# Kernel optimization log

Measured on AMD Instinct MI355X. Metric: run time of the kernel, lower is better.

The kernel has to match this reference:

```python
import jax, jax.numpy as jnp
import numpy as np


def setup_inputs() -> dict:
    key = jax.random.key(0)
    ks = jax.random.split(key, 8)
    B, L, D = 8, 4096, 1024
    s = 1.0 / np.sqrt(D)  # torch Linear default init scale (approx)
    return {
        "x": jax.random.normal(ks[0], (B, L, D), dtype=jnp.float32),
        "hidden": jax.random.normal(ks[1], (B, D), dtype=jnp.float32),
        "W_f": jax.random.normal(ks[2], (D, D), dtype=jnp.float32) * s,
        "b_f": jnp.zeros((D,), dtype=jnp.float32),
        "W_i": jax.random.normal(ks[3], (D, D), dtype=jnp.float32) * s,
        "b_i": jnp.zeros((D,), dtype=jnp.float32),
        "W_o": jax.random.normal(ks[4], (D, D), dtype=jnp.float32) * s,
        "b_o": jnp.zeros((D,), dtype=jnp.float32),
    }


def reference(x, hidden, W_f, b_f, W_i, b_i, W_o, b_o):
    # x: [B, L, D], hidden: [B, D]
    D = x.shape[-1]
    lin = jnp.linspace(0.0, 1.0, D, dtype=x.dtype)  # per-channel gate scale
    remember = jax.nn.sigmoid(jnp.einsum('bld,ed->ble', x, W_f) + b_f) * lin
    forget = 1.0 - remember
    inp = jnp.tanh(jnp.einsum('bld,ed->ble', x, W_i) + b_i) * remember

    # linear recurrence h_t = forget_t * h_{t-1} + inp_t  via parallel scan
    def combine(c1, c2):
        a1, u1 = c1
        a2, u2 = c2
        return (a1 * a2, a2 * u1 + u2)

    cumprod_forget, h_inner = jax.lax.associative_scan(combine, (forget, inp), axis=1)
    h = h_inner + hidden[:, None, :] * cumprod_forget  # inject initial hidden state
    y = jnp.einsum('bld,ed->ble', h, W_o) + b_o
    return y, h
```

## Files before the change

kernel.cpp:

```cpp
#include <hip/hip_runtime.h>
#include <stdint.h>

#define B_ 8
#define L_ 4096
#define D_ 1024
#define M_ (B_*L_)
#define CHUNKS 64
#define TCH (L_/CHUNKS)

typedef float f32x4 __attribute__((ext_vector_type(4)));
typedef float f32x2 __attribute__((ext_vector_type(2)));
typedef short short8 __attribute__((ext_vector_type(8)));
typedef unsigned short ushort4v __attribute__((ext_vector_type(4)));

static __device__ __forceinline__ unsigned short f2bf(float f) {
  union { float f; unsigned u; } v; v.f = f;
  unsigned r = v.u + 0x7FFFu + ((v.u >> 16) & 1u);
  return (unsigned short)(r >> 16);
}
static __device__ __forceinline__ float bf2f(unsigned short u) {
  union { unsigned u; float f; } v; v.u = ((unsigned)u) << 16; return v.f;
}

#define GLOAD16(g, l) \
  __builtin_amdgcn_global_load_lds((__attribute__((address_space(1))) const void*)(g), \
                                   (__attribute__((address_space(3))) void*)(l), 16, 0, 0)

__global__ __launch_bounds__(256)
void cvt_bf16(const float* __restrict__ src, unsigned short* __restrict__ dst, int n8)
{
  int gid = blockIdx.x * 256 + threadIdx.x;
  if (gid >= n8) return;
  const f32x4* s = (const f32x4*)(src + (size_t)gid * 8);
  f32x4 v0 = s[0], v1 = s[1];
  union { short8 v; unsigned short u[8]; } w;
  w.u[0] = f2bf(v0[0]); w.u[1] = f2bf(v0[1]); w.u[2] = f2bf(v0[2]); w.u[3] = f2bf(v0[3]);
  w.u[4] = f2bf(v1[0]); w.u[5] = f2bf(v1[1]); w.u[6] = f2bf(v1[2]); w.u[7] = f2bf(v1[3]);
  *(short8*)(dst + (size_t)gid * 8) = w.v;
}

template<int OBF>
__global__ __launch_bounds__(512, 2)
void gemm256(const unsigned short* __restrict__ A,
             const unsigned short* __restrict__ Bw,
             const float* __restrict__ bias,
             float* __restrict__ outf,
             unsigned short* __restrict__ outb)
{
  __shared__ unsigned short lds[65536];
  char* ldsb = (char*)lds;

  const int tid  = threadIdx.x;
  const int lane = tid & 63;
  const int wid  = tid >> 6;
  const int wm   = wid >> 2;
  const int wn   = wid & 3;
  const int frow = lane & 15, ks = lane >> 4;
  const int xsw  = (ks ^ ((frow >> 1) & 3)) << 4;

  const int nwg = gridDim.x;
  const int wg  = (blockIdx.x & 7) * (nwg >> 3) + (blockIdx.x >> 3);
  const int bm  = (wg & 127) * 256;
  const int bn  = (wg >> 7) * 256;

  const int r0  = tid >> 2;
  const int scl = ((tid & 3) ^ ((r0 >> 1) & 3)) << 4;
  const char* pA = (const char*)A  + (size_t)(bm + r0) * 2048 + scl;
  const char* pB = (const char*)Bw + (size_t)(bn + r0) * 2048 + scl;
  const int dst16 = tid * 16;

  f32x4 acc[8][4] = {};
  short8 aq[4], bq[4];

  auto stgA = [&](int T, int kk, int buf) {
    const char* s = pA + T * 128 + kk * 64;
    char* d = ldsb + buf * 32768 + kk * 16384 + dst16;
    GLOAD16(s, d);
    GLOAD16(s + (size_t)128 * 2048, d + 8192);
  };
  auto stgB = [&](int T, int kk, int buf) {
    const char* s = pB + T * 128 + kk * 64;
    char* d = ldsb + 65536 + buf * 32768 + kk * 16384 + dst16;
    GLOAD16(s, d);
    GLOAD16(s + (size_t)128 * 2048, d + 8192);
  };
  auto ldA4 = [&](const char* LA, int kk, int ih) {
    const char* base = LA + kk * 16384 + (wm * 128 + ih * 64 + frow) * 64 + xsw;
    aq[0] = *(const short8*)(base);
    aq[1] = *(const short8*)(base + 1024);
    aq[2] = *(const short8*)(base + 2048);
    aq[3] = *(const short8*)(base + 3072);
  };
  auto ldB4 = [&](const char* LB, int kk) {
    const char* base = LB + kk * 16384 + (wn * 64 + frow) * 64 + xsw;
    bq[0] = *(const short8*)(base);
    bq[1] = *(const short8*)(base + 1024);
    bq[2] = *(const short8*)(base + 2048);
    bq[3] = *(const short8*)(base + 3072);
  };
  auto mfma16 = [&](int ih) {
    __builtin_amdgcn_s_setprio(1);
    #pragma unroll
    for (int i2 = 0; i2 < 4; ++i2) {
      #pragma unroll
      for (int j = 0; j < 4; ++j)
        acc[ih * 4 + i2][j] =
          __builtin_amdgcn_mfma_f32_16x16x32_bf16(aq[i2], bq[j], acc[ih * 4 + i2][j], 0, 0, 0);
    }
    __builtin_amdgcn_s_setprio(0);
  };

  stgA(0, 0, 0); stgB(0, 0, 0);
  stgA(0, 1, 0); stgB(0, 1, 0);
  stgA(1, 0, 1); stgB(1, 0, 1);
  asm volatile("s_waitcnt vmcnt(8)" ::: "memory");
  __builtin_amdgcn_s_barrier();

  for (int t = 0; t < 16; ++t) {
    const int buf = t & 1;
    const char* LA = ldsb + buf * 32768;
    const char* LB = ldsb + 65536 + buf * 32768;
    ldB4(LB, 0);
    ldA4(LA, 0, 0);
    if (t < 15) stgA(t + 1, 1, (t + 1) & 1);
    __builtin_amdgcn_s_barrier();
    asm volatile("s_waitcnt lgkmcnt(0)" ::: "memory");
    mfma16(0);
    __builtin_amdgcn_s_barrier();
    ldA4(LA, 0, 1);
    if (t < 15) stgB(t + 1, 1, (t + 1) & 1);
    if (t < 15) asm volatile("s_waitcnt vmcnt(8)" ::: "memory");
    else        asm volatile("s_waitcnt vmcnt(0)" ::: "memory");
    __builtin_amdgcn_s_barrier();
    asm volatile("s_waitcnt lgkmcnt(0)" ::: "memory");
    mfma16(1);
    __builtin_amdgcn_s_barrier();
    ldB4(LB, 1);
    ldA4(LA, 1, 0);
    if (t < 14) stgA(t + 2, 0, buf);
    __builtin_amdgcn_s_barrier();
    asm volatile("s_waitcnt lgkmcnt(0)" ::: "memory");
    mfma16(0 + 4 - 4);
    __builtin_amdgcn_s_barrier();
    ldA4(LA, 1, 1);
    if (t < 14) stgB(t + 2, 0, buf);
    if (t < 14) asm volatile("s_waitcnt vmcnt(8)" ::: "memory");
    else        asm volatile("s_waitcnt vmcnt(4)" ::: "memory");
    __builtin_amdgcn_s_barrier();
    asm volatile("s_waitcnt lgkmcnt(0)" ::: "memory");
    mfma16(1);
    __builtin_amdgcn_s_barrier();
  }

  float bv[4];
  #pragma unroll
  for (int j = 0; j < 4; ++j) bv[j] = bias[bn + wn * 64 + j * 16 + frow];
  #pragma unroll
  for (int ii = 0; ii < 8; ++ii) {
    int row = bm + wm * 128 + ii * 16 + ks * 4;
    #pragma unroll
    for (int j = 0; j < 4; ++j) {
      int col = bn + wn * 64 + j * 16 + frow;
      #pragma unroll
      for (int r = 0; r < 4; ++r) {
        float v = acc[ii][j][r] + bv[j];
        if constexpr (OBF) outb[(size_t)(row + r) * D_ + col] = f2bf(v);
        else               outf[(size_t)(row + r) * D_ + col] = v;
      }
    }
  }
}

static __device__ __forceinline__ void gate1(float zf, float zi, float lin,
                                             float& f, float& inp)
{
  float rem = lin / (1.0f + __expf(-zf));
  float ez  = __expf(2.0f * zi);
  float th  = 1.0f - 2.0f / (ez + 1.0f);
  f = 1.0f - rem;
  inp = th * rem;
}

__global__ __launch_bounds__(256)
void scan_partial_b(const unsigned short* __restrict__ zf,
                    const unsigned short* __restrict__ zi,
                    float* __restrict__ Ag, float* __restrict__ Ug)
{
  int blk = blockIdx.x;
  int b = blk >> 6, c = blk & 63;
  int e = threadIdx.x << 2;
  float lin0 = (float)e * (1.0f / 1023.0f);
  size_t base = ((size_t)b * L_ + (size_t)c * TCH) * D_ + e;
  f32x4 a = {1.f,1.f,1.f,1.f}, u = {0.f,0.f,0.f,0.f};
  for (int t = 0; t < TCH; ++t) {
    ushort4v f4 = *(const ushort4v*)(zf + base + (size_t)t * D_);
    ushort4v i4 = *(const ushort4v*)(zi + base + (size_t)t * D_);
    #pragma unroll
    for (int j = 0; j < 4; ++j) {
      float fg, inp;
      gate1(bf2f(f4[j]), bf2f(i4[j]), lin0 + (float)j * (1.0f/1023.0f), fg, inp);
      u[j] = fmaf(fg, u[j], inp);
      a[j] *= fg;
    }
  }
  size_t o = (size_t)(b * CHUNKS + c) * D_ + e;
  *(f32x4*)(Ag + o) = a;
  *(f32x4*)(Ug + o) = u;
}

__global__ __launch_bounds__(256)
void scan_carry(const float* __restrict__ Ag, const float* __restrict__ Ug,
                const float* __restrict__ hidden, float* __restrict__ Hin)
{
  int gid = blockIdx.x * 256 + threadIdx.x;
  int b = gid >> 8;
  int e = (gid & 255) << 2;
  f32x4 h = *(const f32x4*)(hidden + (size_t)b * D_ + e);
  for (int c = 0; c < CHUNKS; ++c) {
    size_t o = (size_t)(b * CHUNKS + c) * D_ + e;
    *(f32x4*)(Hin + o) = h;
    f32x4 A = *(const f32x4*)(Ag + o);
    f32x4 U = *(const f32x4*)(Ug + o);
    h = A * h + U;
  }
}

__global__ __launch_bounds__(256)
void scan_apply_b(const unsigned short* __restrict__ zf,
                  const unsigned short* __restrict__ zi,
                  const float* __restrict__ Hin,
                  float* __restrict__ hout, unsigned short* __restrict__ hb)
{
  int blk = blockIdx.x;
  int b = blk >> 6, c = blk & 63;
  int e = threadIdx.x << 2;
  float lin0 = (float)e * (1.0f / 1023.0f);
  size_t base = ((size_t)b * L_ + (size_t)c * TCH) * D_ + e;
  f32x4 h = *(const f32x4*)(Hin + (size_t)(b * CHUNKS + c) * D_ + e);
  for (int t = 0; t < TCH; ++t) {
    size_t o = base + (size_t)t * D_;
    ushort4v f4 = *(const ushort4v*)(zf + o);
    ushort4v i4 = *(const ushort4v*)(zi + o);
    #pragma unroll
    for (int j = 0; j < 4; ++j) {
      float fg, inp;
      gate1(bf2f(f4[j]), bf2f(i4[j]), lin0 + (float)j * (1.0f/1023.0f), fg, inp);
      h[j] = fmaf(fg, h[j], inp);
    }
    *(f32x4*)(hout + o) = h;
    ushort4v p;
    p[0] = f2bf(h[0]); p[1] = f2bf(h[1]); p[2] = f2bf(h[2]); p[3] = f2bf(h[3]);
    *(ushort4v*)(hb + o) = p;
  }
}

template<int MODE>
__global__ __launch_bounds__(256, 2)
void gemm_slow(const float* __restrict__ A, const float* __restrict__ B0,
               const float* __restrict__ B1, const float* __restrict__ bias0,
               const float* __restrict__ bias1, float* __restrict__ out0,
               float* __restrict__ out1)
{
  constexpr int BK = 32;
  __shared__ unsigned short As[128 * BK];
  __shared__ unsigned short Bs0[128 * BK];
  __shared__ unsigned short Bs1[(MODE == 0) ? (128 * BK) : 8];

  const int tid = threadIdx.x, lane = tid & 63, wave = tid >> 6;
  const int wr = wave >> 1, wc = wave & 1;
  const int bm = blockIdx.x * 128, bn = blockIdx.y * 128;
  f32x4 acc0[4][4] = {};
  f32x4 acc1[(MODE == 0) ? 4 : 1][(MODE == 0) ? 4 : 1] = {};
  const int frow = lane & 15, kslot = lane >> 4;
  const int xs = kslot ^ (frow & 3);

  auto stage = [&](const float* src, unsigned short* dst) {
    #pragma unroll
    for (int p = 0; p < 4; ++p) {
      int g = p * 256 + tid;
      int row = g >> 3, kq = (g & 7) << 2;
      f32x4 v = *(const f32x4*)(src + (size_t)row * D_ + kq);
      ushort4v w;
      w[0] = f2bf(v[0]); w[1] = f2bf(v[1]); w[2] = f2bf(v[2]); w[3] = f2bf(v[3]);
      int byte = kq << 1, slot = byte >> 4, sub = byte & 15;
      int off = row * 64 + ((slot ^ (row & 3)) << 4) + sub;
      *(ushort4v*)((char*)dst + off) = w;
    }
  };

  for (int k0 = 0; k0 < D_; k0 += BK) {
    stage(A + (size_t)bm * D_ + k0, As);
    stage(B0 + (size_t)bn * D_ + k0, Bs0);
    if constexpr (MODE == 0) stage(B1 + (size_t)bn * D_ + k0, Bs1);
    __syncthreads();
    short8 af[4], bf0[4], bf1[4];
    #pragma unroll
    for (int i = 0; i < 4; ++i) {
      int ar = wr * 64 + i * 16 + frow;
      af[i] = *(const short8*)((const char*)As + ar * 64 + (xs << 4));
      int br = wc * 64 + i * 16 + frow;
      bf0[i] = *(const short8*)((const char*)Bs0 + br * 64 + (xs << 4));
      if constexpr (MODE == 0)
        bf1[i] = *(const short8*)((const char*)Bs1 + br * 64 + (xs << 4));
    }
    #pragma unroll
    for (int i = 0; i < 4; ++i)
      #pragma unroll
      for (int j = 0; j < 4; ++j) {
        acc0[i][j] = __builtin_amdgcn_mfma_f32_16x16x32_bf16(af[i], bf0[j], acc0[i][j], 0, 0, 0);
        if constexpr (MODE == 0)
          acc1[i][j] = __builtin_amdgcn_mfma_f32_16x16x32_bf16(af[i], bf1[j], acc1[i][j], 0, 0, 0);
      }
    __syncthreads();
  }
  #pragma unroll
  for (int i = 0; i < 4; ++i)
    #pragma unroll
    for (int j = 0; j < 4; ++j)
      #pragma unroll
      for (int r = 0; r < 4; ++r) {
        int row = bm + wr * 64 + i * 16 + (lane >> 4) * 4 + r;
        int col = bn + wc * 64 + j * 16 + (lane & 15);
        size_t idx = (size_t)row * D_ + col;
        if constexpr (MODE == 0) {
          float zf = acc0[i][j][r] + bias0[col];
          float linv = (float)col * (1.0f / 1023.0f);
          float rem = linv / (1.0f + __expf(-zf));
          float zi = acc1[i][j][r] + bias1[col];
          float e2 = __expf(2.0f * zi);
          float th = 1.0f - 2.0f / (e2 + 1.0f);
          out0[idx] = 1.0f - rem;
          out1[idx] = th * rem;
        } else {
          out0[idx] = acc0[i][j][r] + bias0[col];
        }
      }
}

__global__ __launch_bounds__(256)
void scan_partial_f(const float* __restrict__ p0, const float* __restrict__ p1,
                    float* __restrict__ Ag, float* __restrict__ Ug)
{
  int blk = blockIdx.x;
  int b = blk >> 7;
  int c = (blk >> 1) & (CHUNKS - 1);
  int e = ((blk & 1) << 9) + threadIdx.x * 2;
  size_t base = ((size_t)b * L_ + (size_t)c * TCH) * D_ + e;
  f32x2 a = {1.0f, 1.0f}, u = {0.0f, 0.0f};
  for (int t = 0; t < TCH; ++t) {
    f32x2 f = *(const f32x2*)(p0 + base + (size_t)t * D_);
    f32x2 i = *(const f32x2*)(p1 + base + (size_t)t * D_);
    u = f * u + i;
    a = a * f;
  }
  size_t o = (size_t)(b * CHUNKS + c) * D_ + e;
  *(f32x2*)(Ag + o) = a;
  *(f32x2*)(Ug + o) = u;
}

__global__ __launch_bounds__(256)
void scan_apply_f(const float* __restrict__ p0, float* __restrict__ p1_io,
                  const float* __restrict__ Hin)
{
  int blk = blockIdx.x;
  int b = blk >> 7;
  int c = (blk >> 1) & (CHUNKS - 1);
  int e = ((blk & 1) << 9) + threadIdx.x * 2;
  size_t base = ((size_t)b * L_ + (size_t)c * TCH) * D_ + e;
  f32x2 h = *(const f32x2*)(Hin + (size_t)(b * CHUNKS + c) * D_ + e);
  for (int t = 0; t < TCH; ++t) {
    size_t o = base + (size_t)t * D_;
    f32x2 f = *(const f32x2*)(p0 + o);
    f32x2 i = *(const f32x2*)(p1_io + o);
    h = f * h + i;
    *(f32x2*)(p1_io + o) = h;
  }
}

extern "C" void kernel_launch(void* const* d_in, const int* in_sizes, int n_in,
                              void* d_out, int out_size, void* d_ws, size_t ws_size,
                              hipStream_t stream)
{
  const float* x      = (const float*)d_in[0];
  const float* hidden = (const float*)d_in[1];
  const float* W_f    = (const float*)d_in[2];
  const float* b_f    = (const float*)d_in[3];
  const float* W_i    = (const float*)d_in[4];
  const float* b_i    = (const float*)d_in[5];
  const float* W_o    = (const float*)d_in[6];
  const float* b_o    = (const float*)d_in[7];

  float* y = (float*)d_out;
  float* h = y + (size_t)M_ * D_;

  const size_t xb_elems = (size_t)M_ * D_;
  const size_t w_elems  = (size_t)D_ * D_;
  const size_t agg      = (size_t)B_ * CHUNKS * D_;
  const size_t need = (xb_elems * 3 + 3 * w_elems) * 2 + agg * 3 * 4;

  if (ws_size >= need) {
    unsigned short* xb  = (unsigned short*)d_ws;
    unsigned short* wfb = xb + xb_elems;
    unsigned short* wib = wfb + w_elems;
    unsigned short* wob = wib + w_elems;
    unsigned short* zfb = wob + w_elems;
    unsigned short* zib = zfb + xb_elems;
    float* Ag  = (float*)(zib + xb_elems);
    float* Ug  = Ag + agg;
    float* Hin = Ug + agg;

    cvt_bf16<<<(int)(xb_elems / 8 / 256), 256, 0, stream>>>(x,   xb,  (int)(xb_elems / 8));
    cvt_bf16<<<(int)(w_elems / 8 / 256), 256, 0, stream>>>(W_f, wfb, (int)(w_elems / 8));
    cvt_bf16<<<(int)(w_elems / 8 / 256), 256, 0, stream>>>(W_i, wib, (int)(w_elems / 8));
    cvt_bf16<<<(int)(w_elems / 8 / 256), 256, 0, stream>>>(W_o, wob, (int)(w_elems / 8));

    int gblocks = (M_ / 256) * (D_ / 256);
    gemm256<1><<<gblocks, 512, 0, stream>>>(xb, wfb, b_f, nullptr, zfb);
    gemm256<1><<<gblocks, 512, 0, stream>>>(xb, wib, b_i, nullptr, zib);

    int pblocks = B_ * CHUNKS;
    scan_partial_b<<<pblocks, 256, 0, stream>>>(zfb, zib, Ag, Ug);
    scan_carry<<<(B_ * D_ / 4) / 256, 256, 0, stream>>>(Ag, Ug, hidden, Hin);
    scan_apply_b<<<pblocks, 256, 0, stream>>>(zfb, zib, Hin, h, xb);

    gemm256<0><<<gblocks, 512, 0, stream>>>(xb, wob, b_o, y, nullptr);
  } else {
    float* Ag  = (float*)d_ws;
    float* Ug  = Ag + agg;
    float* Hin = Ug + agg;
    dim3 gg(M_ / 128, D_ / 128);
    int pblocks = B_ * CHUNKS * 2;

    gemm_slow<0><<<gg, 256, 0, stream>>>(x, W_f, W_i, b_f, b_i, y, h);
    scan_partial_f<<<pblocks, 256, 0, stream>>>(y, h, Ag, Ug);
    scan_carry<<<(B_ * D_ / 4) / 256, 256, 0, stream>>>(Ag, Ug, hidden, Hin);
    scan_apply_f<<<pblocks, 256, 0, stream>>>(y, h, Hin);
    gemm_slow<1><<<gg, 256, 0, stream>>>(h, W_o, nullptr, b_o, nullptr, y, nullptr);
  }
}
```

Before: 423.7 us.

## Fuse forget/input GEMMs into one N=2048 GEMM, remap tiles, double scan chunks

The two input-projection GEMMs become a single launch over a concatenated W_f|W_i weight, with each tile writing to the zf or zi plane. x is read once and the output N width doubles. Block-to-tile mapping is redone so each XCD handles a contiguous group of M rows across all N columns, aiming for better L2 reuse. The three weight conversions are merged into one kernel, and the scan chunk count goes from 64 to 128 to give the scan kernels more parallelism. The catch is that the workspace must now hold the three bf16 weights contiguously, and there are more carry steps in the sequential carry kernel.

```diff
diff --git a/kernel.cpp b/kernel.cpp
--- a/kernel.cpp
+++ b/kernel.cpp
@@ -5,7 +5,7 @@
 #define L_ 4096
 #define D_ 1024
 #define M_ (B_*L_)
-#define CHUNKS 64
+#define CHUNKS 128
 #define TCH (L_/CHUNKS)
 
 typedef float f32x4 __attribute__((ext_vector_type(4)));
@@ -39,13 +39,31 @@
   *(short8*)(dst + (size_t)gid * 8) = w.v;
 }
 
-template<int OBF>
+__global__ __launch_bounds__(256)
+void cvt_w3(const float* __restrict__ w0, const float* __restrict__ w1,
+            const float* __restrict__ w2, unsigned short* __restrict__ dst)
+{
+  const int per = (D_ * D_) / 8 / 256;
+  int m = blockIdx.x / per;
+  int gid = (blockIdx.x % per) * 256 + threadIdx.x;
+  const float* src = (m == 0) ? w0 : (m == 1) ? w1 : w2;
+  const f32x4* s = (const f32x4*)(src + (size_t)gid * 8);
+  f32x4 v0 = s[0], v1 = s[1];
+  union { short8 v; unsigned short u[8]; } w;
+  w.u[0] = f2bf(v0[0]); w.u[1] = f2bf(v0[1]); w.u[2] = f2bf(v0[2]); w.u[3] = f2bf(v0[3]);
+  w.u[4] = f2bf(v1[0]); w.u[5] = f2bf(v1[1]); w.u[6] = f2bf(v1[2]); w.u[7] = f2bf(v1[3]);
+  *(short8*)(dst + (size_t)m * D_ * D_ + (size_t)gid * 8) = w.v;
+}
+
+template<int MODE>
 __global__ __launch_bounds__(512, 2)
 void gemm256(const unsigned short* __restrict__ A,
              const unsigned short* __restrict__ Bw,
-             const float* __restrict__ bias,
-             float* __restrict__ outf,
-             unsigned short* __restrict__ outb)
+             const float* __restrict__ bias0,
+             const float* __restrict__ bias1,
+             unsigned short* __restrict__ ob0,
+             unsigned short* __restrict__ ob1,
+             float* __restrict__ of)
 {
   __shared__ unsigned short lds[65536];
   char* ldsb = (char*)lds;
@@ -58,10 +76,14 @@
   const int frow = lane & 15, ks = lane >> 4;
   const int xsw  = (ks ^ ((frow >> 1) & 3)) << 4;
 
-  const int nwg = gridDim.x;
-  const int wg  = (blockIdx.x & 7) * (nwg >> 3) + (blockIdx.x >> 3);
-  const int bm  = (wg & 127) * 256;
-  const int bn  = (wg >> 7) * 256;
+  constexpr int NBN = (MODE == 0) ? 8 : 4;
+  constexpr int GBM = 32 / NBN;
+  const int xcd   = blockIdx.x & 7;
+  const int slot  = blockIdx.x >> 3;
+  const int local = slot & 31;
+  const int wrnd  = slot >> 5;
+  const int bm = (xcd * 16 + wrnd * GBM + (local & (GBM - 1))) * 256;
+  const int bn = (local / GBM) * 256;
 
   const int r0  = tid >> 2;
   const int scl = ((tid & 3) ^ ((r0 >> 1) & 3)) << 4;
@@ -140,7 +162,7 @@
     if (t < 14) stgA(t + 2, 0, buf);
     __builtin_amdgcn_s_barrier();
     asm volatile("s_waitcnt lgkmcnt(0)" ::: "memory");
-    mfma16(0 + 4 - 4);
+    mfma16(0);
     __builtin_amdgcn_s_barrier();
     ldA4(LA, 1, 1);
     if (t < 14) stgB(t + 2, 0, buf);
@@ -152,20 +174,38 @@
     __builtin_amdgcn_s_barrier();
   }
 
-  float bv[4];
-  #pragma unroll
-  for (int j = 0; j < 4; ++j) bv[j] = bias[bn + wn * 64 + j * 16 + frow];
-  #pragma unroll
-  for (int ii = 0; ii < 8; ++ii) {
-    int row = bm + wm * 128 + ii * 16 + ks * 4;
-    #pragma unroll
-    for (int j = 0; j < 4; ++j) {
-      int col = bn + wn * 64 + j * 16 + frow;
+  if constexpr (MODE == 0) {
+    const int plane = bn >> 10;
+    const int cb    = bn & 1023;
+    unsigned short* ob = plane ? ob1 : ob0;
+    const float* bs    = plane ? bias1 : bias0;
+    float bv[4];
+    #pragma unroll
+    for (int j = 0; j < 4; ++j) bv[j] = bs[cb + wn * 64 + j * 16 + frow];
+    #pragma unroll
+    for (int ii = 0; ii < 8; ++ii) {
+      int row = bm + wm * 128 + ii * 16 + ks * 4;
       #pragma unroll
-      for (int r = 0; r < 4; ++r) {
-        float v = acc[ii][j][r] + bv[j];
-        if constexpr (OBF) outb[(size_t)(row + r) * D_ + col] = f2bf(v);
-        else               outf[(size_t)(row + r) * D_ + col] = v;
+      for (int j = 0; j < 4; ++j) {
+        int col = cb + wn * 64 + j * 16 + frow;
+        #pragma unroll
+        for (int r = 0; r < 4; ++r)
+          ob[(size_t)(row + r) * D_ + col] = f2bf(acc[ii][j][r] + bv[j]);
+      }
+    }
+  } else {
+    float bv[4];
+    #pragma unroll
+    for (int j = 0; j < 4; ++j) bv[j] = bias0[bn + wn * 64 + j * 16 + frow];
+    #pragma unroll
+    for (int ii = 0; ii < 8; ++ii) {
+      int row = bm + wm * 128 + ii * 16 + ks * 4;
+      #pragma unroll
+      for (int j = 0; j < 4; ++j) {
+        int col = bn + wn * 64 + j * 16 + frow;
+        #pragma unroll
+        for (int r = 0; r < 4; ++r)
+          of[(size_t)(row + r) * D_ + col] = acc[ii][j][r] + bv[j];
       }
     }
   }
@@ -187,7 +227,7 @@
                     float* __restrict__ Ag, float* __restrict__ Ug)
 {
   int blk = blockIdx.x;
-  int b = blk >> 6, c = blk & 63;
+  int b = blk >> 7, c = blk & (CHUNKS - 1);
   int e = threadIdx.x << 2;
   float lin0 = (float)e * (1.0f / 1023.0f);
   size_t base = ((size_t)b * L_ + (size_t)c * TCH) * D_ + e;
@@ -232,7 +272,7 @@
                   float* __restrict__ hout, unsigned short* __restrict__ hb)
 {
   int blk = blockIdx.x;
-  int b = blk >> 6, c = blk & 63;
+  int b = blk >> 7, c = blk & (CHUNKS - 1);
   int e = threadIdx.x << 2;
   float lin0 = (float)e * (1.0f / 1023.0f);
   size_t base = ((size_t)b * L_ + (size_t)c * TCH) * D_ + e;
@@ -342,7 +382,7 @@
                     float* __restrict__ Ag, float* __restrict__ Ug)
 {
   int blk = blockIdx.x;
-  int b = blk >> 7;
+  int b = blk / (CHUNKS * 2);
   int c = (blk >> 1) & (CHUNKS - 1);
   int e = ((blk & 1) << 9) + threadIdx.x * 2;
   size_t base = ((size_t)b * L_ + (size_t)c * TCH) * D_ + e;
@@ -363,7 +403,7 @@
                   const float* __restrict__ Hin)
 {
   int blk = blockIdx.x;
-  int b = blk >> 7;
+  int b = blk / (CHUNKS * 2);
   int c = (blk >> 1) & (CHUNKS - 1);
   int e = ((blk & 1) << 9) + threadIdx.x * 2;
   size_t base = ((size_t)b * L_ + (size_t)c * TCH) * D_ + e;
@@ -409,21 +449,17 @@
     float* Ug  = Ag + agg;
     float* Hin = Ug + agg;
 
-    cvt_bf16<<<(int)(xb_elems / 8 / 256), 256, 0, stream>>>(x,   xb,  (int)(xb_elems / 8));
-    cvt_bf16<<<(int)(w_elems / 8 / 256), 256, 0, stream>>>(W_f, wfb, (int)(w_elems / 8));
-    cvt_bf16<<<(int)(w_elems / 8 / 256), 256, 0, stream>>>(W_i, wib, (int)(w_elems / 8));
-    cvt_bf16<<<(int)(w_elems / 8 / 256), 256, 0, stream>>>(W_o, wob, (int)(w_elems / 8));
-
-    int gblocks = (M_ / 256) * (D_ / 256);
-    gemm256<1><<<gblocks, 512, 0, stream>>>(xb, wfb, b_f, nullptr, zfb);
-    gemm256<1><<<gblocks, 512, 0, stream>>>(xb, wib, b_i, nullptr, zib);
+    cvt_bf16<<<(int)(xb_elems / 8 / 256), 256, 0, stream>>>(x, xb, (int)(xb_elems / 8));
+    cvt_w3<<<3 * (int)(w_elems / 8 / 256), 256, 0, stream>>>(W_f, W_i, W_o, wfb);
+
+    gemm256<0><<<1024, 512, 0, stream>>>(xb, wfb, b_f, b_i, zfb, zib, nullptr);
 
     int pblocks = B_ * CHUNKS;
     scan_partial_b<<<pblocks, 256, 0, stream>>>(zfb, zib, Ag, Ug);
     scan_carry<<<(B_ * D_ / 4) / 256, 256, 0, stream>>>(Ag, Ug, hidden, Hin);
     scan_apply_b<<<pblocks, 256, 0, stream>>>(zfb, zib, Hin, h, xb);
 
-    gemm256<0><<<gblocks, 512, 0, stream>>>(xb, wob, b_o, y, nullptr);
+    gemm256<1><<<512, 512, 0, stream>>>(xb, wob, b_o, nullptr, nullptr, nullptr, y);
   } else {
     float* Ag  = (float*)d_ws;
     float* Ug  = Ag + agg;
```

New measurement: 390.9 us. 7.7% less time.
